# Performance work log

Hardware: AMD Instinct MI355X
Metric: run time of the kernel (lower is better)

## Reference

```python
import jax, jax.numpy as jnp
import numpy as np

BATCH = 16384
NUM_INPUTS = 4096
NUM_LEAVES = 8192


def setup_inputs() -> dict:
    key = jax.random.key(0)
    kx, ka = jax.random.split(key)
    x = jax.random.normal(kx, (BATCH, NUM_INPUTS), dtype=jnp.float32)
    hard_assignment = jax.random.randint(ka, (NUM_LEAVES,), 0, NUM_INPUTS, dtype=jnp.int64)
    return {"x": x, "hard_assignment": hard_assignment}


def reference(x, hard_assignment):
    # torch: x @ P_hard.T where P_hard[l, hard_assignment[l]] = 1.
    # (x @ P_hard.T)[b, l] = sum_i x[b, i] * P_hard[l, i] = x[b, hard_assignment[l]]
    # => identical math expressed as a column gather (no wasted FLOPs).
    return jnp.take(x, hard_assignment, axis=1)  # [BATCH, NUM_LEAVES]
```

## Files before the change

### kernel.cpp

```cpp
#include <hip/hip_runtime.h>
#include <hip/hip_bf16.h>


#define NUM_INPUTS 4096
#define NUM_LEAVES 8192

__global__ __launch_bounds__(256) void frozenInputToLeaf_gather(
    const float* __restrict__ x,
    const int* __restrict__ idx,
    float* __restrict__ out) {
    __shared__ float row[NUM_INPUTS];

    const int t = threadIdx.x;
    const int b = blockIdx.x;

    const float4* __restrict__ xrow4 = (const float4*)(x + (size_t)b * NUM_INPUTS);
    float4* row4 = (float4*)row;
#pragma unroll
    for (int i = 0; i < 4; ++i) {
        row4[i * 256 + t] = xrow4[i * 256 + t];
    }
    __syncthreads();

    const int4* __restrict__ idx4 = (const int4*)idx;
    float4* __restrict__ out4 = (float4*)(out + (size_t)b * NUM_LEAVES);
#pragma unroll
    for (int i = 0; i < 8; ++i) {
        const int v = i * 256 + t;
        const int4 id = idx4[v];
        float4 r;
        r.x = row[id.x];
        r.y = row[id.y];
        r.z = row[id.z];
        r.w = row[id.w];
        out4[v] = r;
    }
}

extern "C" void kernel_launch(void* const* d_in, const int* in_sizes, int n_in,
                              void* d_out, int out_size, void* d_ws, size_t ws_size,
                              hipStream_t stream) {
    const float* x = (const float*)d_in[0];
    const int* idx = (const int*)d_in[1];
    float* out = (float*)d_out;

    const int batch = in_sizes[0] / NUM_INPUTS;
    frozenInputToLeaf_gather<<<batch, 256, 0, stream>>>(x, idx, out);
}
```

Before: 685.6 us.

## Process eight rows per block with double-buffered async global-to-LDS staging

Each block now handles eight batch rows with 512 threads. The index vectors are loaded once into registers and reused across all eight rows. Rows are staged into a double-buffered LDS array using the global_load_lds builtin, so the load of row r+1 overlaps the gather and store of row r. This is meant to hide global load latency and remove repeated index loads, at the cost of 32KB of LDS per block and a larger block size, which may reduce occupancy. It also depends on the async LDS loads having completed by the time each barrier is reached.

```diff
diff --git a/kernel.cpp b/kernel.cpp
--- a/kernel.cpp
+++ b/kernel.cpp
@@ -1,39 +1,70 @@
 #include <hip/hip_runtime.h>
-#include <hip/hip_bf16.h>
 
 
 #define NUM_INPUTS 4096
 #define NUM_LEAVES 8192
+#define ROWS 8
+#define T 512
 
-__global__ __launch_bounds__(256) void frozenInputToLeaf_gather(
+__device__ __forceinline__ void stage16(const float4* g, float* lds_uniform) {
+    __builtin_amdgcn_global_load_lds(
+        (const __attribute__((address_space(1))) void*)(const void*)g,
+        (__attribute__((address_space(3))) void*)(void*)lds_uniform,
+        16, 0, 0);
+}
+
+__global__ __launch_bounds__(T) void frozenInputToLeaf_gather2(
     const float* __restrict__ x,
     const int* __restrict__ idx,
     float* __restrict__ out) {
-    __shared__ float row[NUM_INPUTS];
+    __shared__ float rows[2][NUM_INPUTS];
 
     const int t = threadIdx.x;
-    const int b = blockIdx.x;
+    const int wave = t >> 6;
+    const int lane = t & 63;
+    const size_t b0 = (size_t)blockIdx.x * ROWS;
 
-    const float4* __restrict__ xrow4 = (const float4*)(x + (size_t)b * NUM_INPUTS);
-    float4* row4 = (float4*)row;
+    int4 id[4];
+    const int4* __restrict__ idx4 = (const int4*)idx;
 #pragma unroll
-    for (int i = 0; i < 4; ++i) {
-        row4[i * 256 + t] = xrow4[i * 256 + t];
+    for (int v = 0; v < 4; ++v) id[v] = idx4[v * T + t];
+
+    {
+        const float4* __restrict__ g = (const float4*)(x + b0 * NUM_INPUTS);
+#pragma unroll
+        for (int j = 0; j < 2; ++j) {
+            const int c = j * 8 + wave;
+            stage16(g + c * 64 + lane, &rows[0][c * 256]);
+        }
     }
     __syncthreads();
 
-    const int4* __restrict__ idx4 = (const int4*)idx;
-    float4* __restrict__ out4 = (float4*)(out + (size_t)b * NUM_LEAVES);
 #pragma unroll
-    for (int i = 0; i < 8; ++i) {
-        const int v = i * 256 + t;
-        const int4 id = idx4[v];
-        float4 r;
-        r.x = row[id.x];
-        r.y = row[id.y];
-        r.z = row[id.z];
-        r.w = row[id.w];
-        out4[v] = r;
+    for (int r = 0; r < ROWS; ++r) {
+        const int cur = r & 1;
+
+        if (r + 1 < ROWS) {
+            const float4* __restrict__ g =
+                (const float4*)(x + (b0 + r + 1) * NUM_INPUTS);
+#pragma unroll
+            for (int j = 0; j < 2; ++j) {
+                const int c = j * 8 + wave;
+                stage16(g + c * 64 + lane, &rows[cur ^ 1][c * 256]);
+            }
+        }
+
+        float4* __restrict__ o4 = (float4*)(out + (b0 + r) * NUM_LEAVES);
+#pragma unroll
+        for (int v = 0; v < 4; ++v) {
+            float4 o;
+            o.x = rows[cur][id[v].x];
+            o.y = rows[cur][id[v].y];
+            o.z = rows[cur][id[v].z];
+            o.w = rows[cur][id[v].w];
+            o4[v * T + t] = o;
+        }
+
+        __syncthreads();
     }
 }
 
@@ -45,5 +76,5 @@
     float* out = (float*)d_out;
 
     const int batch = in_sizes[0] / NUM_INPUTS;
-    frozenInputToLeaf_gather<<<batch, 256, 0, stream>>>(x, idx, out);
+    frozenInputToLeaf_gather2<<<batch / ROWS, T, 0, stream>>>(x, idx, out);
 }
```

Result: no change. 691.0 us (+0.8%).
